# Optimization experiments

Measured on AMD Instinct MI355X. Metric: run time of the kernel, lower is better.

Reference implementation:

```python
import jax, jax.numpy as jnp
import numpy as np

M, LAM, MAX_ITER, TOL, BETA = 5, 1e-4, 50, 0.01, 1.0


def anderson_fixed_point(lin_w, lin_b, x0):
    """Anderson acceleration for x = Linear(x), faithful to the torch loop.
    x0: (bsz, d, H, W); the fixed-point map applies the linear over W."""
    bsz = x0.shape[0]
    n = x0.size // bsz
    shape = x0.shape
    dt = x0.dtype

    def f(v_flat):  # (bsz, n) -> (bsz, n)
        return (v_flat.reshape(shape) @ lin_w.T + lin_b).reshape(bsz, n)

    x0f = x0.reshape(bsz, n)
    F0 = f(x0f)
    X = jnp.zeros((bsz, M, n), dt).at[:, 0].set(x0f).at[:, 1].set(F0)
    Fm = jnp.zeros((bsz, M, n), dt).at[:, 0].set(F0).at[:, 1].set(f(F0))
    y = jnp.zeros((bsz, M + 1), dt).at[:, 0].set(1.0)
    eyeM = jnp.eye(M, dtype=dt)

    def cond(c):
        _, _, k, res = c
        return (k < MAX_ITER) & (res >= TOL)

    def body(c):
        X, Fm, k, _ = c
        nk = jnp.minimum(k, M)
        # mask inactive history slots (k < M early iterations); padded rows/cols
        # get lam on the diagonal and 0 border -> alpha_j = 0 there, identical
        # to torch's solve on the leading (n+1)x(n+1) submatrix.
        mask = (jnp.arange(M) < nk).astype(dt)               # (M,)
        G = (Fm - X) * mask[None, :, None]                   # (bsz, M, n)
        Hin = jnp.einsum('bin,bjn->bij', G, G) + LAM * eyeM  # (bsz, M, M)
        H = jnp.zeros((bsz, M + 1, M + 1), dt)
        H = H.at[:, 0, 1:].set(mask).at[:, 1:, 0].set(mask).at[:, 1:, 1:].set(Hin)
        alpha = jnp.linalg.solve(H, y[..., None])[:, 1:, 0]  # (bsz, M)
        xnew = BETA * jnp.einsum('bm,bmn->bn', alpha, Fm) + (1.0 - BETA) * jnp.einsum('bm,bmn->bn', alpha, X)
        idx = k % M
        X = X.at[:, idx].set(xnew)
        fnew = f(xnew)
        Fm = Fm.at[:, idx].set(fnew)
        res = jnp.linalg.norm(fnew - xnew) / (1e-5 + jnp.linalg.norm(fnew))
        return (X, Fm, k + 1, res)

    Xf, _, kf, _ = jax.lax.while_loop(
        cond, body, (X, Fm, jnp.int32(2), jnp.asarray(jnp.inf, dt)))
    return Xf[:, (kf - 1) % M].reshape(shape)


def setup_inputs() -> dict:
    key = jax.random.key(0)
    k1, k2, k3, k4, k5 = jax.random.split(key, 5)
    B, D, H, W = 16, 8, 128, 512  # in_features = out_features = W = 512
    x = jax.random.normal(k1, (B, D, H, W), jnp.float32)
    # contractive inner linear so the fixed-point iteration behaves
    lin_w = jax.random.normal(k2, (W, W), jnp.float32) * 0.02
    lin_b = jax.random.normal(k3, (W,), jnp.float32) * 0.1
    weight = jax.random.normal(k4, (W, W), jnp.float32) * 0.02
    bias = jax.random.normal(k5, (W,), jnp.float32) * 0.1
    return {"x": x, "lin_w": lin_w, "lin_b": lin_b, "weight": weight, "bias": bias}


def reference(x, lin_w, lin_b, weight, bias):
    # torch runs the solver under no_grad -> stop_gradient for fidelity
    x_star = anderson_fixed_point(
        jax.lax.stop_gradient(lin_w),
        jax.lax.stop_gradient(lin_b),
        jax.lax.stop_gradient(x))
    return x_star @ weight.T + bias
```

## Files before the change

kernel.cpp:

```cpp
#include <hip/hip_runtime.h>
#include <math.h>

#define FD     512
#define NBATCH 16
#define NROWS  16384
#define ROWS   32
#define NBLK   (NROWS/ROWS)
#define TPB    512
#define MM     5
#define LAMV   1e-4f
#define MAXIT  50
#define TOLV   0.01f
#define NTOT   8388608
#define PADW   520

typedef __attribute__((ext_vector_type(8))) short  short8;
typedef __attribute__((ext_vector_type(4))) float  float4v;

__device__ unsigned short g_Fm[MM][NTOT];
__device__ unsigned short g_G [MM][NTOT];
__device__ unsigned short g_xb[NTOT];
__device__ unsigned short g_Wb [FD*FD];
__device__ unsigned short g_WbO[FD*FD];
__device__ float g_acc [MAXIT-2][NBATCH][8];
__device__ float g_acc0[NBATCH][8];

static __device__ __forceinline__ unsigned short f2bf(float f) {
    unsigned u = __float_as_uint(f);
    u += 0x7fff + ((u >> 16) & 1);
    return (unsigned short)(u >> 16);
}
static __device__ __forceinline__ float bf2f(unsigned short s) {
    return __uint_as_float(((unsigned)s) << 16);
}

template<int MODE>
static __device__ __forceinline__ void mfma_gemm(const unsigned short* __restrict__ Wb,
                                                 const float* __restrict__ bvec,
                                                 const unsigned short* AsIn,
                                                 unsigned short* FsOut,
                                                 float* __restrict__ gout)
{
    const int lane = threadIdx.x & 63;
    const int wv   = threadIdx.x >> 6;
    const int lm   = lane & 15;
    const int quad = lane >> 4;
    float4v acc[2][4];
#pragma unroll
    for (int ct = 0; ct < 4; ct++) {
        const float b = bvec[(wv*4+ct)*16 + lm];
        acc[0][ct][0]=b; acc[0][ct][1]=b; acc[0][ct][2]=b; acc[0][ct][3]=b;
        acc[1][ct][0]=b; acc[1][ct][1]=b; acc[1][ct][2]=b; acc[1][ct][3]=b;
    }
#pragma unroll
    for (int q = 0; q < 4; q++) {
        short8 af[2][4];
#pragma unroll
        for (int r16 = 0; r16 < 2; r16++)
#pragma unroll
            for (int kb = 0; kb < 4; kb++)
                af[r16][kb] = *(const short8*)(AsIn + (r16*16 + lm)*PADW + q*128 + kb*32 + quad*8);
#pragma unroll
        for (int ct = 0; ct < 4; ct++) {
            const unsigned short* bp = Wb + ((wv*4+ct)*16 + lm)*FD + q*128 + quad*8;
            const short8 b0 = *(const short8*)(bp);
            const short8 b1 = *(const short8*)(bp + 32);
            const short8 b2 = *(const short8*)(bp + 64);
            const short8 b3 = *(const short8*)(bp + 96);
            acc[0][ct] = __builtin_amdgcn_mfma_f32_16x16x32_bf16(af[0][0], b0, acc[0][ct], 0,0,0);
            acc[1][ct] = __builtin_amdgcn_mfma_f32_16x16x32_bf16(af[1][0], b0, acc[1][ct], 0,0,0);
            acc[0][ct] = __builtin_amdgcn_mfma_f32_16x16x32_bf16(af[0][1], b1, acc[0][ct], 0,0,0);
            acc[1][ct] = __builtin_amdgcn_mfma_f32_16x16x32_bf16(af[1][1], b1, acc[1][ct], 0,0,0);
            acc[0][ct] = __builtin_amdgcn_mfma_f32_16x16x32_bf16(af[0][2], b2, acc[0][ct], 0,0,0);
            acc[1][ct] = __builtin_amdgcn_mfma_f32_16x16x32_bf16(af[1][2], b2, acc[1][ct], 0,0,0);
            acc[0][ct] = __builtin_amdgcn_mfma_f32_16x16x32_bf16(af[0][3], b3, acc[0][ct], 0,0,0);
            acc[1][ct] = __builtin_amdgcn_mfma_f32_16x16x32_bf16(af[1][3], b3, acc[1][ct], 0,0,0);
        }
    }
#pragma unroll
    for (int ct = 0; ct < 4; ct++) {
        const int c = (wv*4+ct)*16 + lm;
#pragma unroll
        for (int r16 = 0; r16 < 2; r16++)
#pragma unroll
            for (int r = 0; r < 4; r++) {
                const int row = r16*16 + quad*4 + r;
                if (MODE == 0) FsOut[row*PADW + c] = f2bf(acc[r16][ct][r]);
                else           gout[row*FD + c]    = acc[r16][ct][r];
            }
    }
}

static __device__ __forceinline__ void red6(const float vals[6], float (*redS)[8], float* accrow)
{
    const int lane = threadIdx.x & 63, wv = threadIdx.x >> 6;
#pragma unroll
    for (int j = 0; j < 6; j++) {
        float v = vals[j];
#pragma unroll
        for (int o = 32; o; o >>= 1) v += __shfl_down(v, o);
        if (lane == 0) redS[wv][j] = v;
    }
    __syncthreads();
    if (threadIdx.x < 6) {
        float s = 0.f;
#pragma unroll
        for (int w = 0; w < 8; w++) s += redS[w][threadIdx.x];
        atomicAdd(accrow + threadIdx.x, s);
    }
}

__global__ void __launch_bounds__(256) k_init0(const float* __restrict__ lin_w,
                                               const float* __restrict__ weight)
{
    const int i0 = blockIdx.x*256 + threadIdx.x, stride = gridDim.x*256;
    for (int i = i0; i < FD*FD; i += stride) {
        g_Wb [i] = f2bf(lin_w[i]);
        g_WbO[i] = f2bf(weight[i]);
    }
    float* a = &g_acc[0][0][0];
    for (int i = i0; i < (MAXIT-2)*NBATCH*8; i += stride) a[i] = 0.f;
    float* a0 = &g_acc0[0][0];
    for (int i = i0; i < NBATCH*8; i += stride) a0[i] = 0.f;
}

__global__ void __launch_bounds__(TPB, 4) k_init1(const float* __restrict__ x,
                                                  const float* __restrict__ lin_b)
{
    __shared__ __align__(16) unsigned short As[ROWS*PADW];
    __shared__ __align__(16) unsigned short Fs[ROWS*PADW];
    __shared__ float redS[8][8];
    const int tid = threadIdx.x;
    const int t = blockIdx.x, b = t >> 5;
    const int base = t * (ROWS*FD);

#pragma unroll
    for (int i = 0; i < 4; i++) {
        const int e = (i*TPB + tid) * 8;
        const float4 a0 = *(const float4*)(x + base + e);
        const float4 a1 = *(const float4*)(x + base + e + 4);
        short8 v;
        v[0]=f2bf(a0.x); v[1]=f2bf(a0.y); v[2]=f2bf(a0.z); v[3]=f2bf(a0.w);
        v[4]=f2bf(a1.x); v[5]=f2bf(a1.y); v[6]=f2bf(a1.z); v[7]=f2bf(a1.w);
        *(short8*)(As + (e>>9)*PADW + (e&511)) = v;
    }
    __syncthreads();
    mfma_gemm<0>(g_Wb, lin_b, As, Fs, nullptr);
    __syncthreads();
    float d00 = 0.f;
#pragma unroll
    for (int i = 0; i < 4; i++) {
        const int e = (i*TPB + tid) * 8;
        const int off = base + e, lo = (e>>9)*PADW + (e&511);
        const short8 fv = *(const short8*)(Fs + lo);
        const short8 xv = *(const short8*)(As + lo);
        short8 gv;
#pragma unroll
        for (int j = 0; j < 8; j++) {
            const float g = bf2f((unsigned short)fv[j]) - bf2f((unsigned short)xv[j]);
            gv[j] = (short)f2bf(g);
            d00 = fmaf(g, g, d00);
        }
        *(short8*)(&g_Fm[0][off]) = fv;
        *(short8*)(&g_G [0][off]) = gv;
    }
    __syncthreads();
    mfma_gemm<0>(g_Wb, lin_b, Fs, As, nullptr);
    __syncthreads();
    float d01 = 0.f, d11 = 0.f;
#pragma unroll
    for (int i = 0; i < 4; i++) {
        const int e = (i*TPB + tid) * 8;
        const int off = base + e, lo = (e>>9)*PADW + (e&511);
        const short8 f1 = *(const short8*)(As + lo);
        const short8 f0 = *(const short8*)(Fs + lo);
        const short8 g0 = *(const short8*)(&g_G[0][off]);
        short8 gv;
#pragma unroll
        for (int j = 0; j < 8; j++) {
            const float g = bf2f((unsigned short)f1[j]) - bf2f((unsigned short)f0[j]);
            gv[j] = (short)f2bf(g);
            d11 = fmaf(g, g, d11);
            d01 = fmaf(bf2f((unsigned short)g0[j]), g, d01);
        }
        *(short8*)(&g_Fm[1][off]) = f1;
        *(short8*)(&g_G [1][off]) = gv;
    }
    const float vals[6] = {d00, d01, d11, 0.f, 0.f, 0.f};
    red6(vals, redS, &g_acc0[b][0]);
}

__global__ void __launch_bounds__(TPB, 4) k_iter(const float* __restrict__ lin_b, int k)
{
    __shared__ __align__(16) unsigned short As[ROWS*PADW];
    __shared__ __align__(16) unsigned short Fs[ROWS*PADW];
    __shared__ float gramS[MM][MM];
    __shared__ float alphaS[MM];
    __shared__ float Hs[48];
    __shared__ float redS[8][8];
    __shared__ float sres;

    const int tid = threadIdx.x;
    const int t = blockIdx.x, b = t >> 5;
    const int base = t * (ROWS*FD);
    const int it = k - 2, idx = k % MM, nk = (k < MM) ? k : MM;

    if (k > 2) {
        float v = 0.f;
        if (tid < 32) {
            const int bb = tid & 15;
            const int jj = (tid < 16) ? ((k-1) % MM) : 5;
            v = g_acc[it-1][bb][jj];
        }
        v += __shfl_xor(v, 1); v += __shfl_xor(v, 2);
        v += __shfl_xor(v, 4); v += __shfl_xor(v, 8);
        const float num = __shfl(v, 0), den = __shfl(v, 16);
        if (tid == 0) sres = sqrtf(num) / (1e-5f + sqrtf(den));
    }
    __syncthreads();
    if (k > 2 && sres < TOLV) return;

    if (tid == 0) {
#pragma unroll
        for (int i = 0; i < MM; i++)
#pragma unroll
            for (int j = 0; j < MM; j++) gramS[i][j] = 0.f;
        gramS[0][0] = g_acc0[b][0];
        gramS[0][1] = gramS[1][0] = g_acc0[b][1];
        gramS[1][1] = g_acc0[b][2];
        const int j0 = (k - 5 > 2) ? (k - 5) : 2;
        for (int j = j0; j < k; j++) {
            const int ij = j % MM, nkj = (j < MM) ? j : MM;
            for (int c = 0; c < MM; c++)
                if (c < nkj || c == ij) {
                    const float vv = g_acc[j-2][b][c];
                    gramS[ij][c] = vv; gramS[c][ij] = vv;
                }
        }
        float* H = Hs;
        for (int i = 0; i < 42; i++) H[i] = 0.f;
        for (int j = 0; j < nk; j++) { H[1+j] = 1.f; H[(1+j)*7] = 1.f; }
#pragma unroll
        for (int i = 0; i < MM; i++) H[(1+i)*7 + (1+i)] = LAMV;
        for (int i = 0; i < nk; i++)
            for (int j = 0; j < nk; j++)
                H[(1+i)*7 + (1+j)] = gramS[i][j] + (i == j ? LAMV : 0.f);
        H[6] = 1.f;
        for (int col = 0; col < 6; col++) {
            int p = col; float mx = fabsf(H[col*7+col]);
            for (int r2 = col+1; r2 < 6; r2++) {
                const float vv = fabsf(H[r2*7+col]);
                if (vv > mx) { mx = vv; p = r2; }
            }
            if (p != col)
                for (int j = col; j < 7; j++) { const float tt = H[col*7+j]; H[col*7+j] = H[p*7+j]; H[p*7+j] = tt; }
            const float piv = H[col*7+col];
            for (int r2 = col+1; r2 < 6; r2++) {
                const float fct = H[r2*7+col] / piv;
                for (int j = col+1; j < 7; j++) H[r2*7+j] -= fct * H[col*7+j];
            }
        }
        for (int r2 = 5; r2 >= 0; r2--) {
            float s = H[r2*7+6];
            for (int j = r2+1; j < 6; j++) s -= H[r2*7+j] * H[j*7+6];
            H[r2*7+6] = s / H[r2*7+r2];
        }
#pragma unroll
        for (int m = 0; m < MM; m++) alphaS[m] = H[(1+m)*7+6];
    }
    __syncthreads();

    float al[MM];
#pragma unroll
    for (int m = 0; m < MM; m++) al[m] = alphaS[m];

    if (nk == MM) {
#pragma unroll
        for (int i = 0; i < 4; i++) {
            const int e = (i*TPB + tid) * 8;
            const int off = base + e;
            float s[8] = {0,0,0,0,0,0,0,0};
#pragma unroll
            for (int m = 0; m < MM; m++) {
                const short8 fm = *(const short8*)(&g_Fm[m][off]);
#pragma unroll
                for (int j = 0; j < 8; j++)
                    s[j] = fmaf(al[m], bf2f((unsigned short)fm[j]), s[j]);
            }
            short8 v;
#pragma unroll
            for (int j = 0; j < 8; j++) v[j] = (short)f2bf(s[j]);
            *(short8*)(As + (e>>9)*PADW + (e&511)) = v;
            *(short8*)(&g_xb[off]) = v;
        }
    } else {
#pragma unroll
        for (int i = 0; i < 4; i++) {
            const int e = (i*TPB + tid) * 8;
            const int off = base + e;
            float s[8] = {0,0,0,0,0,0,0,0};
            for (int m = 0; m < nk; m++) {
                const short8 fm = *(const short8*)(&g_Fm[m][off]);
#pragma unroll
                for (int j = 0; j < 8; j++)
                    s[j] = fmaf(al[m], bf2f((unsigned short)fm[j]), s[j]);
            }
            short8 v;
#pragma unroll
            for (int j = 0; j < 8; j++) v[j] = (short)f2bf(s[j]);
            *(short8*)(As + (e>>9)*PADW + (e&511)) = v;
            *(short8*)(&g_xb[off]) = v;
        }
    }
    __syncthreads();
    mfma_gemm<0>(g_Wb, lin_b, As, Fs, nullptr);
    __syncthreads();
    float dv[6] = {0,0,0,0,0,0};
    float dself = 0.f;
#pragma unroll
    for (int i = 0; i < 4; i++) {
        const int e = (i*TPB + tid) * 8;
        const int off = base + e, lo = (e>>9)*PADW + (e&511);
        const short8 fv = *(const short8*)(Fs + lo);
        const short8 xv = *(const short8*)(As + lo);
        float gg[8]; short8 gv;
#pragma unroll
        for (int j = 0; j < 8; j++) {
            const float ff = bf2f((unsigned short)fv[j]);
            const float g  = ff - bf2f((unsigned short)xv[j]);
            gg[j] = g; gv[j] = (short)f2bf(g);
            dv[5] = fmaf(ff, ff, dv[5]);
            dself = fmaf(g, g, dself);
        }
        *(short8*)(&g_Fm[idx][off]) = fv;
        *(short8*)(&g_G [idx][off]) = gv;
#pragma unroll
        for (int js = 0; js < MM; js++) {
            if (js != idx && js < nk) {
                const short8 gj = *(const short8*)(&g_G[js][off]);
#pragma unroll
                for (int j = 0; j < 8; j++)
                    dv[js] = fmaf(gg[j], bf2f((unsigned short)gj[j]), dv[js]);
            }
        }
    }
    float vals[6];
#pragma unroll
    for (int j = 0; j < MM; j++) vals[j] = (j == idx) ? (dv[j] + dself) : dv[j];
    vals[5] = dv[5];
    red6(vals, redS, &g_acc[it][b][0]);
}

__global__ void __launch_bounds__(TPB, 4) k_final(const float* __restrict__ bias,
                                                  float* __restrict__ out)
{
    __shared__ __align__(16) unsigned short As[ROWS*PADW];
    const int tid = threadIdx.x;
    const int base = blockIdx.x * (ROWS*FD);
#pragma unroll
    for (int i = 0; i < 4; i++) {
        const int e = (i*TPB + tid) * 8;
        *(short8*)(As + (e>>9)*PADW + (e&511)) = *(const short8*)(&g_xb[base + e]);
    }
    __syncthreads();
    mfma_gemm<1>(g_WbO, bias, As, nullptr, out + base);
}

extern "C" void kernel_launch(void* const* d_in, const int* in_sizes, int n_in,
                              void* d_out, int out_size, void* d_ws, size_t ws_size,
                              hipStream_t stream)
{
    (void)in_sizes; (void)n_in; (void)out_size; (void)d_ws; (void)ws_size;
    const float* x      = (const float*)d_in[0];
    const float* lin_w  = (const float*)d_in[1];
    const float* lin_b  = (const float*)d_in[2];
    const float* weight = (const float*)d_in[3];
    const float* bias   = (const float*)d_in[4];
    float* out = (float*)d_out;

    hipLaunchKernelGGL(k_init0, dim3(512),  dim3(256), 0, stream, lin_w, weight);
    hipLaunchKernelGGL(k_init1, dim3(NBLK), dim3(TPB), 0, stream, x, lin_b);
    for (int k = 2; k < MAXIT; k++)
        hipLaunchKernelGGL(k_iter, dim3(NBLK), dim3(TPB), 0, stream, lin_b, k);
    hipLaunchKernelGGL(k_final, dim3(NBLK), dim3(TPB), 0, stream, bias, out);
}
```

Before: 732.3 us.

## Double rows per block and restructure MFMA tiling for weight reuse

Rows per block go from 32 to 64 and threads per block from 512 to 1024, so each batch now spans 16 blocks instead of 32. The GEMM is rearranged so each wave owns 32 output columns across four 16-row tiles. Each loaded weight fragment now feeds four MFMAs, which cuts global weight traffic per row. The cost is that LDS per block roughly doubles, fewer blocks can be resident per CU, and the unchanged launch-bounds occupancy hint with 1024 threads may squeeze registers and cause spills.

```diff
diff --git a/kernel.cpp b/kernel.cpp
--- a/kernel.cpp
+++ b/kernel.cpp
@@ -4,9 +4,9 @@
 #define FD     512
 #define NBATCH 16
 #define NROWS  16384
-#define ROWS   32
+#define ROWS   64
 #define NBLK   (NROWS/ROWS)
-#define TPB    512
+#define TPB    1024
 #define MM     5
 #define LAMV   1e-4f
 #define MAXIT  50
@@ -45,43 +45,40 @@
     const int wv   = threadIdx.x >> 6;
     const int lm   = lane & 15;
     const int quad = lane >> 4;
-    float4v acc[2][4];
-#pragma unroll
-    for (int ct = 0; ct < 4; ct++) {
-        const float b = bvec[(wv*4+ct)*16 + lm];
-        acc[0][ct][0]=b; acc[0][ct][1]=b; acc[0][ct][2]=b; acc[0][ct][3]=b;
-        acc[1][ct][0]=b; acc[1][ct][1]=b; acc[1][ct][2]=b; acc[1][ct][3]=b;
+    float4v acc[4][2];
+#pragma unroll
+    for (int ct = 0; ct < 2; ct++) {
+        const float b = bvec[wv*32 + ct*16 + lm];
+#pragma unroll
+        for (int r16 = 0; r16 < 4; r16++) {
+            acc[r16][ct][0]=b; acc[r16][ct][1]=b; acc[r16][ct][2]=b; acc[r16][ct][3]=b;
+        }
     }
 #pragma unroll
     for (int q = 0; q < 4; q++) {
-        short8 af[2][4];
-#pragma unroll
-        for (int r16 = 0; r16 < 2; r16++)
-#pragma unroll
-            for (int kb = 0; kb < 4; kb++)
-                af[r16][kb] = *(const short8*)(AsIn + (r16*16 + lm)*PADW + q*128 + kb*32 + quad*8);
-#pragma unroll
-        for (int ct = 0; ct < 4; ct++) {
-            const unsigned short* bp = Wb + ((wv*4+ct)*16 + lm)*FD + q*128 + quad*8;
-            const short8 b0 = *(const short8*)(bp);
-            const short8 b1 = *(const short8*)(bp + 32);
-            const short8 b2 = *(const short8*)(bp + 64);
-            const short8 b3 = *(const short8*)(bp + 96);
-            acc[0][ct] = __builtin_amdgcn_mfma_f32_16x16x32_bf16(af[0][0], b0, acc[0][ct], 0,0,0);
-            acc[1][ct] = __builtin_amdgcn_mfma_f32_16x16x32_bf16(af[1][0], b0, acc[1][ct], 0,0,0);
-            acc[0][ct] = __builtin_amdgcn_mfma_f32_16x16x32_bf16(af[0][1], b1, acc[0][ct], 0,0,0);
-            acc[1][ct] = __builtin_amdgcn_mfma_f32_16x16x32_bf16(af[1][1], b1, acc[1][ct], 0,0,0);
-            acc[0][ct] = __builtin_amdgcn_mfma_f32_16x16x32_bf16(af[0][2], b2, acc[0][ct], 0,0,0);
-            acc[1][ct] = __builtin_amdgcn_mfma_f32_16x16x32_bf16(af[1][2], b2, acc[1][ct], 0,0,0);
-            acc[0][ct] = __builtin_amdgcn_mfma_f32_16x16x32_bf16(af[0][3], b3, acc[0][ct], 0,0,0);
-            acc[1][ct] = __builtin_amdgcn_mfma_f32_16x16x32_bf16(af[1][3], b3, acc[1][ct], 0,0,0);
-        }
-    }
-#pragma unroll
-    for (int ct = 0; ct < 4; ct++) {
-        const int c = (wv*4+ct)*16 + lm;
-#pragma unroll
-        for (int r16 = 0; r16 < 2; r16++)
+#pragma unroll
+        for (int kb = 0; kb < 4; kb++) {
+            const int ko = q*128 + kb*32 + quad*8;
+            short8 bf[2];
+#pragma unroll
+            for (int ct = 0; ct < 2; ct++)
+                bf[ct] = *(const short8*)(Wb + (wv*32 + ct*16 + lm)*FD + ko);
+            short8 af[4];
+#pragma unroll
+            for (int r16 = 0; r16 < 4; r16++)
+                af[r16] = *(const short8*)(AsIn + (r16*16 + lm)*PADW + ko);
+#pragma unroll
+            for (int r16 = 0; r16 < 4; r16++) {
+                acc[r16][0] = __builtin_amdgcn_mfma_f32_16x16x32_bf16(af[r16], bf[0], acc[r16][0], 0,0,0);
+                acc[r16][1] = __builtin_amdgcn_mfma_f32_16x16x32_bf16(af[r16], bf[1], acc[r16][1], 0,0,0);
+            }
+        }
+    }
+#pragma unroll
+    for (int ct = 0; ct < 2; ct++) {
+        const int c = wv*32 + ct*16 + lm;
+#pragma unroll
+        for (int r16 = 0; r16 < 4; r16++)
 #pragma unroll
             for (int r = 0; r < 4; r++) {
                 const int row = r16*16 + quad*4 + r;
@@ -105,7 +102,7 @@
     if (threadIdx.x < 6) {
         float s = 0.f;
 #pragma unroll
-        for (int w = 0; w < 8; w++) s += redS[w][threadIdx.x];
+        for (int w = 0; w < 16; w++) s += redS[w][threadIdx.x];
         atomicAdd(accrow + threadIdx.x, s);
     }
 }
@@ -129,9 +126,9 @@
 {
     __shared__ __align__(16) unsigned short As[ROWS*PADW];
     __shared__ __align__(16) unsigned short Fs[ROWS*PADW];
-    __shared__ float redS[8][8];
+    __shared__ float redS[16][8];
     const int tid = threadIdx.x;
-    const int t = blockIdx.x, b = t >> 5;
+    const int t = blockIdx.x, b = t >> 4;
     const int base = t * (ROWS*FD);
 
 #pragma unroll
@@ -197,11 +194,11 @@
     __shared__ float gramS[MM][MM];
     __shared__ float alphaS[MM];
     __shared__ float Hs[48];
-    __shared__ float redS[8][8];
+    __shared__ float redS[16][8];
     __shared__ float sres;
 
     const int tid = threadIdx.x;
-    const int t = blockIdx.x, b = t >> 5;
+    const int t = blockIdx.x, b = t >> 4;
     const int base = t * (ROWS*FD);
     const int it = k - 2, idx = k % MM, nk = (k < MM) ? k : MM;
 
```

Result: faster. 630.0 us (-14.0%).
